# Kernel tuning notes

Hardware: AMD Instinct MI355X
Metric: run time of the kernel (lower is better)

Reference implementation:

```python
import jax, jax.numpy as jnp
import numpy as np

N = 50000          # nodes
E = 400000         # random edges (self-loops added in reference, per PyG default)
IN, HID, HEADS, OUT = 20, 64, 4, 256
NEG_SLOPE = 0.2    # GATv2Conv default negative_slope
EPS = 1e-16        # PyG softmax denom epsilon


def setup_inputs() -> dict:
    key = jax.random.key(0)
    ks = jax.random.split(key, 14)
    g = lambda k, shape, scale=0.1: (jax.random.normal(k, shape, jnp.float32) * scale)
    return {
        "x": jax.random.normal(ks[0], (N, IN), jnp.float32),
        "edge_index": jax.random.randint(ks[1], (2, E), 0, N, jnp.int32),
        # layer 1: GATv2Conv(IN -> HID, heads=HEADS, concat=True)
        "W_l1": g(ks[2], (IN, HEADS * HID)),
        "b_l1": jnp.zeros((HEADS * HID,), jnp.float32),
        "W_r1": g(ks[3], (IN, HEADS * HID)),
        "b_r1": jnp.zeros((HEADS * HID,), jnp.float32),
        "att1": g(ks[4], (HEADS, HID)),
        "bias1": jnp.zeros((HEADS * HID,), jnp.float32),
        # layer 2: GATv2Conv(HEADS*HID -> OUT, heads=1, concat=False)
        "W_l2": g(ks[5], (HEADS * HID, OUT)),
        "b_l2": jnp.zeros((OUT,), jnp.float32),
        "W_r2": g(ks[6], (HEADS * HID, OUT)),
        "b_r2": jnp.zeros((OUT,), jnp.float32),
        "att2": g(ks[7], (1, OUT)),
        "bias2": jnp.zeros((OUT,), jnp.float32),
    }


def _gatv2_layer(x, src, dst, W_l, b_l, W_r, b_r, att, bias, heads, ch, concat):
    n = x.shape[0]
    x_l = (x @ W_l + b_l).reshape(n, heads, ch)  # source transform
    x_r = (x @ W_r + b_r).reshape(n, heads, ch)  # target transform
    # GATv2: e_ij = att . LeakyReLU(x_l[j] + x_r[i])   (j->i edge)
    pre = jax.nn.leaky_relu(x_l[src] + x_r[dst], NEG_SLOPE)       # [E, H, C]
    logits = jnp.einsum('ehc,hc->eh', pre, att)                    # [E, H]
    # segment softmax over destination node (self-loops guarantee nonempty)
    m = jax.ops.segment_max(logits, dst, num_segments=n)
    w = jnp.exp(logits - m[dst])
    denom = jax.ops.segment_sum(w, dst, num_segments=n)
    alpha = w / (denom[dst] + EPS)                                 # [E, H]
    out = jax.ops.segment_sum(x_l[src] * alpha[:, :, None], dst, num_segments=n)
    out = out.reshape(n, heads * ch) if concat else out.mean(axis=1)
    return out + bias


def reference(x, edge_index, W_l1, b_l1, W_r1, b_r1, att1, bias1,
              W_l2, b_l2, W_r2, b_r2, att2, bias2):
    n = x.shape[0]
    loop = jnp.arange(n, dtype=edge_index.dtype)  # PyG add_self_loops=True
    src = jnp.concatenate([edge_index[0], loop])
    dst = jnp.concatenate([edge_index[1], loop])
    h = _gatv2_layer(x, src, dst, W_l1, b_l1, W_r1, b_r1, att1, bias1, HEADS, HID, True)
    h = jax.nn.elu(h)
    out = _gatv2_layer(h, src, dst, W_l2, b_l2, W_r2, b_r2, att2, bias2, 1, OUT, False)
    return out
```

## Files before the change

### kernel.cpp

```cpp
#include <hip/hip_runtime.h>
#include <math.h>

#define CH 256
#define SCAN_BLOCK 1024

typedef _Float16 h2 __attribute__((ext_vector_type(2)));
typedef _Float16 h4 __attribute__((ext_vector_type(4)));
typedef _Float16 f16x8 __attribute__((ext_vector_type(8)));
typedef float f32x4 __attribute__((ext_vector_type(4)));

__device__ __forceinline__ float elu(float v)   { return v > 0.f ? v : __expf(v) - 1.f; }

__device__ __forceinline__ unsigned short f2h(float f) {
    union { _Float16 h; unsigned short u; } c;
    c.h = (_Float16)f;
    return c.u;
}

__device__ __forceinline__ float edge_logit(h4 r, h2 xrlo, h2 xrhi, h2 alo, h2 ahi) {
    const h2 k = {(_Float16)0.2f, (_Float16)0.2f};
    h2 rlo = {r.x, r.y}, rhi = {r.z, r.w};
    h2 slo = rlo + xrlo;
    h2 shi = rhi + xrhi;
    slo = __builtin_elementwise_max(slo, slo * k);
    shi = __builtin_elementwise_max(shi, shi * k);
    float p = __builtin_amdgcn_fdot2(slo, alo, 0.f, false);
    return __builtin_amdgcn_fdot2(shi, ahi, p, false);
}

typedef const __attribute__((address_space(1))) unsigned int* gas_p;
typedef __attribute__((address_space(3))) unsigned int* las_p;
__device__ __forceinline__ void gload16(const unsigned short* g, unsigned short* l) {
    __builtin_amdgcn_global_load_lds((gas_p)g, (las_p)l, 16, 0, 0);
}

__global__ __launch_bounds__(256) void gemm1_kernel(const float* __restrict__ x,
                             const float* __restrict__ Wl, const float* __restrict__ bl,
                             const float* __restrict__ Wr, const float* __restrict__ br,
                             unsigned short* __restrict__ xl, unsigned short* __restrict__ xr, int n) {
    __shared__ float xs[64][20];
    int n0 = blockIdx.x * 64;
    int tid = threadIdx.x;
    for (int i = tid; i < 64 * 20; i += 256) {
        int m = i / 20, k = i % 20;
        int row = n0 + m;
        xs[m][k] = (row < n) ? x[(size_t)row * 20 + k] : 0.f;
    }
    int c = tid;
    float wl[20], wr[20];
#pragma unroll
    for (int k = 0; k < 20; ++k) { wl[k] = Wl[k * 256 + c]; wr[k] = Wr[k * 256 + c]; }
    float blv = bl[c], brv = br[c];
    __syncthreads();
#pragma unroll 1
    for (int g = 0; g < 8; ++g) {
        int base = g * 8;
        float al[8], ar[8];
#pragma unroll
        for (int m = 0; m < 8; ++m) { al[m] = blv; ar[m] = brv; }
#pragma unroll
        for (int k = 0; k < 20; ++k) {
            float wlv = wl[k], wrv = wr[k];
#pragma unroll
            for (int m = 0; m < 8; ++m) {
                float xv = xs[base + m][k];
                al[m] += xv * wlv;
                ar[m] += xv * wrv;
            }
        }
#pragma unroll
        for (int m = 0; m < 8; ++m) {
            int row = n0 + base + m;
            if (row < n) {
                xl[(size_t)row * 256 + c] = f2h(al[m]);
                xr[(size_t)row * 256 + c] = f2h(ar[m]);
            }
        }
    }
}

__global__ void count_deg(const int* __restrict__ ei, int* __restrict__ deg, int e) {
    int t = blockIdx.x * blockDim.x + threadIdx.x;
    if (t < e) atomicAdd(&deg[ei[e + t]], 1);
}

__global__ void scan_block_k(const int* __restrict__ deg, int* __restrict__ rowptr,
                             int* __restrict__ bsums, int n) {
    __shared__ int wsum[16];
    __shared__ int woff[17];
    int tid = threadIdx.x;
    int gi = blockIdx.x * SCAN_BLOCK + tid;
    int lane = tid & 63, wid = tid >> 6;
    int v = (gi < n) ? deg[gi] : 0;
    int incl = v;
#pragma unroll
    for (int d = 1; d < 64; d <<= 1) {
        int t = __shfl_up(incl, d, 64);
        if (lane >= d) incl += t;
    }
    if (lane == 63) wsum[wid] = incl;
    __syncthreads();
    if (tid < 16) {
        int s = wsum[tid];
#pragma unroll
        for (int d = 1; d < 16; d <<= 1) {
            int t = __shfl_up(s, d, 64);
            if (tid >= d) s += t;
        }
        woff[tid + 1] = s;
        if (tid == 0) woff[0] = 0;
    }
    __syncthreads();
    incl += woff[wid];
    if (gi < n) rowptr[gi + 1] = incl;
    if (tid == 0) bsums[blockIdx.x] = woff[16];
}

__global__ void scan_tops_k(int* bsums, int nb) {
    int tid = threadIdx.x;
    int v = (tid < nb) ? bsums[tid] : 0;
    int incl = v;
#pragma unroll
    for (int d = 1; d < 64; d <<= 1) {
        int t = __shfl_up(incl, d, 64);
        if (tid >= d) incl += t;
    }
    if (tid < nb) bsums[tid] = incl - v;
}

__global__ void scan_fix_k(int* __restrict__ rowptr, int* __restrict__ cursor,
                           const int* __restrict__ deg, const int* __restrict__ bsums, int n) {
    int gi = blockIdx.x * SCAN_BLOCK + threadIdx.x;
    if (gi >= n) return;
    int off = bsums[blockIdx.x];
    int incl = rowptr[gi + 1] + off;
    rowptr[gi + 1] = incl;
    cursor[gi] = incl - deg[gi];
    if (gi == 0) rowptr[0] = 0;
}

__global__ void scatter_k(const int* __restrict__ ei, int* __restrict__ cursor,
                          int* __restrict__ csr, int e) {
    int t = blockIdx.x * blockDim.x + threadIdx.x;
    if (t >= e) return;
    int s = ei[t], d = ei[e + t];
    int idx = atomicAdd(&cursor[d], 1);
    csr[idx] = s;
}

__global__ void fused_gat1(const unsigned short* __restrict__ xl, const unsigned short* __restrict__ xr,
                           const int* __restrict__ rowptr, const int* __restrict__ csr,
                           const float* __restrict__ att, const float* __restrict__ bias,
                           unsigned short* __restrict__ hout, int n) {
    int wid = threadIdx.x >> 6;
    int lane = threadIdx.x & 63;
    int i = blockIdx.x * 4 + wid;
    if (i >= n) return;
    h4 xr4 = ((const h4*)(xr + (size_t)i * CH))[lane];
    h2 xrlo = {xr4.x, xr4.y}, xrhi = {xr4.z, xr4.w};
    float4 a4 = ((const float4*)att)[lane];
    h2 alo = {(_Float16)a4.x, (_Float16)a4.y};
    h2 ahi = {(_Float16)a4.z, (_Float16)a4.w};
    h4 xli = ((const h4*)(xl + (size_t)i * CH))[lane];
    float ps = edge_logit(xli, xrlo, xrhi, alo, ahi);
    ps += __shfl_xor(ps, 1); ps += __shfl_xor(ps, 2);
    ps += __shfl_xor(ps, 4); ps += __shfl_xor(ps, 8);
    float m = ps, l = 1.f;
    float4 acc = make_float4((float)xli.x, (float)xli.y, (float)xli.z, (float)xli.w);
    int beg = rowptr[i], end = rowptr[i + 1];
    for (int e = beg; e < end; e += 4) {
        int cnt = end - e;
        int s0 = csr[e];
        int s1 = (cnt > 1) ? csr[e + 1] : s0;
        int s2 = (cnt > 2) ? csr[e + 2] : s0;
        int s3 = (cnt > 3) ? csr[e + 3] : s0;
        h4 r0 = ((const h4*)(xl + (size_t)s0 * CH))[lane];
        h4 r1 = ((const h4*)(xl + (size_t)s1 * CH))[lane];
        h4 r2 = ((const h4*)(xl + (size_t)s2 * CH))[lane];
        h4 r3 = ((const h4*)(xl + (size_t)s3 * CH))[lane];
        float p0 = edge_logit(r0, xrlo, xrhi, alo, ahi);
        float p1 = edge_logit(r1, xrlo, xrhi, alo, ahi);
        float p2 = edge_logit(r2, xrlo, xrhi, alo, ahi);
        float p3 = edge_logit(r3, xrlo, xrhi, alo, ahi);
        p0 += __shfl_xor(p0, 1); p1 += __shfl_xor(p1, 1); p2 += __shfl_xor(p2, 1); p3 += __shfl_xor(p3, 1);
        p0 += __shfl_xor(p0, 2); p1 += __shfl_xor(p1, 2); p2 += __shfl_xor(p2, 2); p3 += __shfl_xor(p3, 2);
        p0 += __shfl_xor(p0, 4); p1 += __shfl_xor(p1, 4); p2 += __shfl_xor(p2, 4); p3 += __shfl_xor(p3, 4);
        p0 += __shfl_xor(p0, 8); p1 += __shfl_xor(p1, 8); p2 += __shfl_xor(p2, 8); p3 += __shfl_xor(p3, 8);
        if (cnt < 2) p1 = -INFINITY;
        if (cnt < 3) p2 = -INFINITY;
        if (cnt < 4) p3 = -INFINITY;
        float mn = fmaxf(m, fmaxf(fmaxf(p0, p1), fmaxf(p2, p3)));
        float sc = __expf(m - mn);
        float w0 = __expf(p0 - mn), w1 = __expf(p1 - mn);
        float w2 = __expf(p2 - mn), w3 = __expf(p3 - mn);
        l = l * sc + w0 + w1 + w2 + w3;
        acc.x = acc.x * sc + w0 * (float)r0.x + w1 * (float)r1.x + w2 * (float)r2.x + w3 * (float)r3.x;
        acc.y = acc.y * sc + w0 * (float)r0.y + w1 * (float)r1.y + w2 * (float)r2.y + w3 * (float)r3.y;
        acc.z = acc.z * sc + w0 * (float)r0.z + w1 * (float)r1.z + w2 * (float)r2.z + w3 * (float)r3.z;
        acc.w = acc.w * sc + w0 * (float)r0.w + w1 * (float)r1.w + w2 * (float)r2.w + w3 * (float)r3.w;
        m = mn;
    }
    float inv = 1.f / (l + 1e-16f);
    float4 b4 = ((const float4*)bias)[lane];
    h4 o;
    o.x = (_Float16)elu(acc.x * inv + b4.x);
    o.y = (_Float16)elu(acc.y * inv + b4.y);
    o.z = (_Float16)elu(acc.z * inv + b4.z);
    o.w = (_Float16)elu(acc.w * inv + b4.w);
    ((h4*)(hout + (size_t)i * CH))[lane] = o;
}

__global__ void fused_gat2(const unsigned short* __restrict__ xl, const unsigned short* __restrict__ xr,
                           const int* __restrict__ rowptr, const int* __restrict__ csr,
                           const float* __restrict__ att, const float* __restrict__ bias,
                           float* __restrict__ out, int n) {
    int wid = threadIdx.x >> 6;
    int lane = threadIdx.x & 63;
    int i = blockIdx.x * 4 + wid;
    if (i >= n) return;
    h4 xr4 = ((const h4*)(xr + (size_t)i * CH))[lane];
    h2 xrlo = {xr4.x, xr4.y}, xrhi = {xr4.z, xr4.w};
    float4 a4 = ((const float4*)att)[lane];
    h2 alo = {(_Float16)a4.x, (_Float16)a4.y};
    h2 ahi = {(_Float16)a4.z, (_Float16)a4.w};
    h4 xli = ((const h4*)(xl + (size_t)i * CH))[lane];
    float ps = edge_logit(xli, xrlo, xrhi, alo, ahi);
    ps += __shfl_xor(ps, 1); ps += __shfl_xor(ps, 2); ps += __shfl_xor(ps, 4);
    ps += __shfl_xor(ps, 8); ps += __shfl_xor(ps, 16); ps += __shfl_xor(ps, 32);
    float m = ps, l = 1.f;
    float4 acc = make_float4((float)xli.x, (float)xli.y, (float)xli.z, (float)xli.w);
    int beg = rowptr[i], end = rowptr[i + 1];
    for (int e = beg; e < end; e += 4) {
        int cnt = end - e;
        int s0 = csr[e];
        int s1 = (cnt > 1) ? csr[e + 1] : s0;
        int s2 = (cnt > 2) ? csr[e + 2] : s0;
        int s3 = (cnt > 3) ? csr[e + 3] : s0;
        h4 r0 = ((const h4*)(xl + (size_t)s0 * CH))[lane];
        h4 r1 = ((const h4*)(xl + (size_t)s1 * CH))[lane];
        h4 r2 = ((const h4*)(xl + (size_t)s2 * CH))[lane];
        h4 r3 = ((const h4*)(xl + (size_t)s3 * CH))[lane];
        float p0 = edge_logit(r0, xrlo, xrhi, alo, ahi);
        float p1 = edge_logit(r1, xrlo, xrhi, alo, ahi);
        float p2 = edge_logit(r2, xrlo, xrhi, alo, ahi);
        float p3 = edge_logit(r3, xrlo, xrhi, alo, ahi);
#pragma unroll
        for (int d = 1; d < 64; d <<= 1) {
            p0 += __shfl_xor(p0, d); p1 += __shfl_xor(p1, d);
            p2 += __shfl_xor(p2, d); p3 += __shfl_xor(p3, d);
        }
        if (cnt < 2) p1 = -INFINITY;
        if (cnt < 3) p2 = -INFINITY;
        if (cnt < 4) p3 = -INFINITY;
        float mn = fmaxf(m, fmaxf(fmaxf(p0, p1), fmaxf(p2, p3)));
        float sc = __expf(m - mn);
        float w0 = __expf(p0 - mn), w1 = __expf(p1 - mn);
        float w2 = __expf(p2 - mn), w3 = __expf(p3 - mn);
        l = l * sc + w0 + w1 + w2 + w3;
        acc.x = acc.x * sc + w0 * (float)r0.x + w1 * (float)r1.x + w2 * (float)r2.x + w3 * (float)r3.x;
        acc.y = acc.y * sc + w0 * (float)r0.y + w1 * (float)r1.y + w2 * (float)r2.y + w3 * (float)r3.y;
        acc.z = acc.z * sc + w0 * (float)r0.z + w1 * (float)r1.z + w2 * (float)r2.z + w3 * (float)r3.z;
        acc.w = acc.w * sc + w0 * (float)r0.w + w1 * (float)r1.w + w2 * (float)r2.w + w3 * (float)r3.w;
        m = mn;
    }
    float inv = 1.f / (l + 1e-16f);
    float4 b4 = ((const float4*)bias)[lane];
    float4 o;
    o.x = acc.x * inv + b4.x;
    o.y = acc.y * inv + b4.y;
    o.z = acc.z * inv + b4.z;
    o.w = acc.w * inv + b4.w;
    ((float4*)(out + (size_t)i * CH))[lane] = o;
}

__global__ void wconv(const float* __restrict__ Wl2, const float* __restrict__ Wr2,
                      unsigned short* __restrict__ Wt) {
    int t = blockIdx.x * 256 + threadIdx.x;
    int z = t >> 16;
    int idx = t & 65535;
    int k = idx >> 8, nn = idx & 255;
    const float* W = z ? Wr2 : Wl2;
    Wt[z * 65536 + nn * 256 + k] = f2h(W[k * 256 + nn]);
}

#define LDE 32
__global__ __launch_bounds__(256) void gemm_mfma(
        const unsigned short* __restrict__ A,
        const unsigned short* __restrict__ Wt,
        const float* __restrict__ ba, const float* __restrict__ bb,
        unsigned short* __restrict__ Ca, unsigned short* __restrict__ Cb, int M) {
    const unsigned short* Wz = Wt + (size_t)blockIdx.z * 65536;
    const float* bias = blockIdx.z ? bb : ba;
    unsigned short* C = blockIdx.z ? Cb : Ca;

    __shared__ unsigned short As[2][128 * LDE];
    __shared__ unsigned short Bs[2][128 * LDE];

    int m0 = blockIdx.x * 128, n0 = blockIdx.y * 128;
    int tid = threadIdx.x;
    int lane = tid & 63, wid = tid >> 6;
    int wm = wid & 1, wn = wid >> 1;
    int q = lane >> 4, l15 = lane & 15;

    int lr = lane >> 2;
    int lc = (lane & 3) * 8;
    int Mm1 = M - 1;
    int ra0 = m0 + wid * 32 + lr;      if (ra0 > Mm1) ra0 = Mm1;
    int ra1 = m0 + wid * 32 + 16 + lr; if (ra1 > Mm1) ra1 = Mm1;
    const unsigned short* pa0 = A  + (size_t)ra0 * 256 + lc;
    const unsigned short* pa1 = A  + (size_t)ra1 * 256 + lc;
    const unsigned short* pb0 = Wz + (size_t)(n0 + wid * 32 + lr) * 256 + lc;
    const unsigned short* pb1 = Wz + (size_t)(n0 + wid * 32 + 16 + lr) * 256 + lc;

    f32x4 acc[4][4];
#pragma unroll
    for (int i = 0; i < 4; ++i)
#pragma unroll
        for (int j = 0; j < 4; ++j) acc[i][j] = (f32x4){0.f, 0.f, 0.f, 0.f};

#define STAGE(b, kb) do {                                   \
        int koff = (kb) * 32;                               \
        gload16(pa0 + koff, &As[b][(wid * 32) * LDE]);      \
        gload16(pa1 + koff, &As[b][(wid * 32 + 16) * LDE]); \
        gload16(pb0 + koff, &Bs[b][(wid * 32) * LDE]);      \
        gload16(pb1 + koff, &Bs[b][(wid * 32 + 16) * LDE]); \
    } while (0)

    STAGE(0, 0);
    __syncthreads();

#pragma unroll
    for (int kb = 0; kb < 8; ++kb) {
        int cur = kb & 1;
        if (kb < 7) STAGE(cur ^ 1, kb + 1);

        f16x8 af[4], bfr[4];
#pragma unroll
        for (int f = 0; f < 4; ++f)
            af[f] = *(const f16x8*)&As[cur][(wm * 64 + f * 16 + l15) * LDE + q * 8];
#pragma unroll
        for (int f = 0; f < 4; ++f)
            bfr[f] = *(const f16x8*)&Bs[cur][(wn * 64 + f * 16 + l15) * LDE + q * 8];
#pragma unroll
        for (int i = 0; i < 4; ++i)
#pragma unroll
            for (int j = 0; j < 4; ++j)
                acc[i][j] = __builtin_amdgcn_mfma_f32_16x16x32_f16(af[i], bfr[j], acc[i][j], 0, 0, 0);

        __syncthreads();
    }
#undef STAGE

#pragma unroll
    for (int j = 0; j < 4; ++j) {
        int gcol = n0 + wn * 64 + j * 16 + l15;
        float bcol = bias[gcol];
#pragma unroll
        for (int i = 0; i < 4; ++i) {
            int row = m0 + wm * 64 + i * 16 + q * 4;
#pragma unroll
            for (int rr = 0; rr < 4; ++rr) {
                int grow = row + rr;
                if (grow < M)
                    C[(size_t)grow * 256 + gcol] = f2h(acc[i][j][rr] + bcol);
            }
        }
    }
}

extern "C" void kernel_launch(void* const* d_in, const int* in_sizes, int n_in,
                              void* d_out, int out_size, void* d_ws, size_t ws_size,
                              hipStream_t stream) {
    const float* x    = (const float*)d_in[0];
    const int*   ei   = (const int*)d_in[1];
    const float* Wl1  = (const float*)d_in[2];
    const float* bl1  = (const float*)d_in[3];
    const float* Wr1  = (const float*)d_in[4];
    const float* br1  = (const float*)d_in[5];
    const float* att1 = (const float*)d_in[6];
    const float* bias1= (const float*)d_in[7];
    const float* Wl2  = (const float*)d_in[8];
    const float* bl2  = (const float*)d_in[9];
    const float* Wr2  = (const float*)d_in[10];
    const float* br2  = (const float*)d_in[11];
    const float* att2 = (const float*)d_in[12];
    const float* bias2= (const float*)d_in[13];

    int n = in_sizes[0] / 20;
    int e = in_sizes[1] / 2;
    float* out = (float*)d_out;
    size_t nch = (size_t)n * CH;

    unsigned short* buf0 = (unsigned short*)d_ws;
    unsigned short* buf1 = buf0 + nch;
    unsigned short* hbuf = buf1 + nch;
    unsigned short* wt2  = hbuf + nch;
    int* deg    = (int*)(wt2 + 2 * 65536);
    int* rowptr = deg + n;
    int* cursor = rowptr + n + 1;
    int* bsums  = cursor + n;
    int* csr    = bsums + 64;

    hipMemsetAsync(deg, 0, (size_t)n * sizeof(int), stream);

    gemm1_kernel<<<(n + 63) / 64, 256, 0, stream>>>(x, Wl1, bl1, Wr1, br1, buf0, buf1, n);

    count_deg<<<(e + 255) / 256, 256, 0, stream>>>(ei, deg, e);
    int nb = (n + SCAN_BLOCK - 1) / SCAN_BLOCK;
    scan_block_k<<<nb, SCAN_BLOCK, 0, stream>>>(deg, rowptr, bsums, n);
    scan_tops_k<<<1, 64, 0, stream>>>(bsums, nb);
    scan_fix_k<<<nb, SCAN_BLOCK, 0, stream>>>(rowptr, cursor, deg, bsums, n);
    scatter_k<<<(e + 255) / 256, 256, 0, stream>>>(ei, cursor, csr, e);

    wconv<<<512, 256, 0, stream>>>(Wl2, Wr2, wt2);

    fused_gat1<<<(n + 3) / 4, 256, 0, stream>>>(buf0, buf1, rowptr, csr, att1, bias1, hbuf, n);

    gemm_mfma<<<dim3((n + 127) / 128, 2, 2), 256, 0, stream>>>(hbuf, wt2, bl2, br2, buf0, buf1, n);

    fused_gat2<<<(n + 3) / 4, 256, 0, stream>>>(buf0, buf1, rowptr, csr, att2, bias2, out, n);
}
```

Before: 315.9 us.

## Unroll edge gathers to 8, use DPP reductions and exp2 online softmax

Both fused GAT aggregation kernels now gather eight neighbour rows per iteration instead of four, which raises memory-level parallelism on the random xl gathers. Intra-16-lane logit reductions use DPP row operations instead of ds_swizzle/bpermute shuffles. The attention vector is pre-scaled by log2(e) so the softmax can use exp2 directly, and the running-max rescale is skipped when the max does not change. In exchange, register pressure rises and tail iterations do redundant loads of the last valid edge; fp16 rounding of the prescaled attention weights changes results slightly.

```diff
diff --git a/kernel.cpp b/kernel.cpp
--- a/kernel.cpp
+++ b/kernel.cpp
@@ -3,6 +3,7 @@
 
 #define CH 256
 #define SCAN_BLOCK 1024
+#define LOG2E 1.44269504088896f
 
 typedef _Float16 h2 __attribute__((ext_vector_type(2)));
 typedef _Float16 h4 __attribute__((ext_vector_type(4)));
@@ -26,6 +27,25 @@
     shi = __builtin_elementwise_max(shi, shi * k);
     float p = __builtin_amdgcn_fdot2(slo, alo, 0.f, false);
     return __builtin_amdgcn_fdot2(shi, ahi, p, false);
+}
+
+template<int C>
+__device__ __forceinline__ float dppadd(float v) {
+    int t = __builtin_amdgcn_update_dpp(0, __float_as_int(v), C, 0xf, 0xf, true);
+    return v + __int_as_float(t);
+}
+__device__ __forceinline__ float red16(float p) {
+    p = dppadd<0xB1>(p);
+    p = dppadd<0x4E>(p);
+    p = dppadd<0x141>(p);
+    p = dppadd<0x140>(p);
+    return p;
+}
+__device__ __forceinline__ float red64(float p) {
+    p = red16(p);
+    p += __shfl_xor(p, 16);
+    p += __shfl_xor(p, 32);
+    return p;
 }
 
 typedef const __attribute__((address_space(1))) unsigned int* gas_p;
@@ -159,46 +179,69 @@
     h4 xr4 = ((const h4*)(xr + (size_t)i * CH))[lane];
     h2 xrlo = {xr4.x, xr4.y}, xrhi = {xr4.z, xr4.w};
     float4 a4 = ((const float4*)att)[lane];
-    h2 alo = {(_Float16)a4.x, (_Float16)a4.y};
-    h2 ahi = {(_Float16)a4.z, (_Float16)a4.w};
+    h2 alo = {(_Float16)(a4.x * LOG2E), (_Float16)(a4.y * LOG2E)};
+    h2 ahi = {(_Float16)(a4.z * LOG2E), (_Float16)(a4.w * LOG2E)};
     h4 xli = ((const h4*)(xl + (size_t)i * CH))[lane];
-    float ps = edge_logit(xli, xrlo, xrhi, alo, ahi);
-    ps += __shfl_xor(ps, 1); ps += __shfl_xor(ps, 2);
-    ps += __shfl_xor(ps, 4); ps += __shfl_xor(ps, 8);
-    float m = ps, l = 1.f;
+    float m = red16(edge_logit(xli, xrlo, xrhi, alo, ahi));
+    float l = 1.f;
     float4 acc = make_float4((float)xli.x, (float)xli.y, (float)xli.z, (float)xli.w);
     int beg = rowptr[i], end = rowptr[i + 1];
-    for (int e = beg; e < end; e += 4) {
+    int el = end - 1;
+    for (int e = beg; e < end; e += 8) {
         int cnt = end - e;
         int s0 = csr[e];
-        int s1 = (cnt > 1) ? csr[e + 1] : s0;
-        int s2 = (cnt > 2) ? csr[e + 2] : s0;
-        int s3 = (cnt > 3) ? csr[e + 3] : s0;
+        int s1 = csr[min(e + 1, el)];
+        int s2 = csr[min(e + 2, el)];
+        int s3 = csr[min(e + 3, el)];
+        int s4 = csr[min(e + 4, el)];
+        int s5 = csr[min(e + 5, el)];
+        int s6 = csr[min(e + 6, el)];
+        int s7 = csr[min(e + 7, el)];
         h4 r0 = ((const h4*)(xl + (size_t)s0 * CH))[lane];
         h4 r1 = ((const h4*)(xl + (size_t)s1 * CH))[lane];
         h4 r2 = ((const h4*)(xl + (size_t)s2 * CH))[lane];
         h4 r3 = ((const h4*)(xl + (size_t)s3 * CH))[lane];
-        float p0 = edge_logit(r0, xrlo, xrhi, alo, ahi);
-        float p1 = edge_logit(r1, xrlo, xrhi, alo, ahi);
-        float p2 = edge_logit(r2, xrlo, xrhi, alo, ahi);
-        float p3 = edge_logit(r3, xrlo, xrhi, alo, ahi);
-        p0 += __shfl_xor(p0, 1); p1 += __shfl_xor(p1, 1); p2 += __shfl_xor(p2, 1); p3 += __shfl_xor(p3, 1);
-        p0 += __shfl_xor(p0, 2); p1 += __shfl_xor(p1, 2); p2 += __shfl_xor(p2, 2); p3 += __shfl_xor(p3, 2);
-        p0 += __shfl_xor(p0, 4); p1 += __shfl_xor(p1, 4); p2 += __shfl_xor(p2, 4); p3 += __shfl_xor(p3, 4);
-        p0 += __shfl_xor(p0, 8); p1 += __shfl_xor(p1, 8); p2 += __shfl_xor(p2, 8); p3 += __shfl_xor(p3, 8);
-        if (cnt < 2) p1 = -INFINITY;
-        if (cnt < 3) p2 = -INFINITY;
-        if (cnt < 4) p3 = -INFINITY;
-        float mn = fmaxf(m, fmaxf(fmaxf(p0, p1), fmaxf(p2, p3)));
-        float sc = __expf(m - mn);
-        float w0 = __expf(p0 - mn), w1 = __expf(p1 - mn);
-        float w2 = __expf(p2 - mn), w3 = __expf(p3 - mn);
-        l = l * sc + w0 + w1 + w2 + w3;
-        acc.x = acc.x * sc + w0 * (float)r0.x + w1 * (float)r1.x + w2 * (float)r2.x + w3 * (float)r3.x;
-        acc.y = acc.y * sc + w0 * (float)r0.y + w1 * (float)r1.y + w2 * (float)r2.y + w3 * (float)r3.y;
-        acc.z = acc.z * sc + w0 * (float)r0.z + w1 * (float)r1.z + w2 * (float)r2.z + w3 * (float)r3.z;
-        acc.w = acc.w * sc + w0 * (float)r0.w + w1 * (float)r1.w + w2 * (float)r2.w + w3 * (float)r3.w;
-        m = mn;
+        h4 r4 = ((const h4*)(xl + (size_t)s4 * CH))[lane];
+        h4 r5 = ((const h4*)(xl + (size_t)s5 * CH))[lane];
+        h4 r6 = ((const h4*)(xl + (size_t)s6 * CH))[lane];
+        h4 r7 = ((const h4*)(xl + (size_t)s7 * CH))[lane];
+        float p0 = red16(edge_logit(r0, xrlo, xrhi, alo, ahi));
+        float p1 = red16(edge_logit(r1, xrlo, xrhi, alo, ahi));
+        float p2 = red16(edge_logit(r2, xrlo, xrhi, alo, ahi));
+        float p3 = red16(edge_logit(r3, xrlo, xrhi, alo, ahi));
+        float p4 = red16(edge_logit(r4, xrlo, xrhi, alo, ahi));
+        float p5 = red16(edge_logit(r5, xrlo, xrhi, alo, ahi));
+        float p6 = red16(edge_logit(r6, xrlo, xrhi, alo, ahi));
+        float p7 = red16(edge_logit(r7, xrlo, xrhi, alo, ahi));
+        if (cnt < 8) {
+            if (cnt <= 1) p1 = -INFINITY;
+            if (cnt <= 2) p2 = -INFINITY;
+            if (cnt <= 3) p3 = -INFINITY;
+            if (cnt <= 4) p4 = -INFINITY;
+            if (cnt <= 5) p5 = -INFINITY;
+            if (cnt <= 6) p6 = -INFINITY;
+            p7 = -INFINITY;
+        }
+        float mn = fmaxf(m, fmaxf(fmaxf(fmaxf(p0, p1), fmaxf(p2, p3)),
+                                  fmaxf(fmaxf(p4, p5), fmaxf(p6, p7))));
+        if (mn > m) {
+            float sc = __builtin_exp2f(m - mn);
+            l *= sc; acc.x *= sc; acc.y *= sc; acc.z *= sc; acc.w *= sc;
+            m = mn;
+        }
+        float w0 = __builtin_exp2f(p0 - m), w1 = __builtin_exp2f(p1 - m);
+        float w2 = __builtin_exp2f(p2 - m), w3 = __builtin_exp2f(p3 - m);
+        float w4 = __builtin_exp2f(p4 - m), w5 = __builtin_exp2f(p5 - m);
+        float w6 = __builtin_exp2f(p6 - m), w7 = __builtin_exp2f(p7 - m);
+        l += ((w0 + w1) + (w2 + w3)) + ((w4 + w5) + (w6 + w7));
+        acc.x += w0*(float)r0.x + w1*(float)r1.x + w2*(float)r2.x + w3*(float)r3.x
+               + w4*(float)r4.x + w5*(float)r5.x + w6*(float)r6.x + w7*(float)r7.x;
+        acc.y += w0*(float)r0.y + w1*(float)r1.y + w2*(float)r2.y + w3*(float)r3.y
+               + w4*(float)r4.y + w5*(float)r5.y + w6*(float)r6.y + w7*(float)r7.y;
+        acc.z += w0*(float)r0.z + w1*(float)r1.z + w2*(float)r2.z + w3*(float)r3.z
+               + w4*(float)r4.z + w5*(float)r5.z + w6*(float)r6.z + w7*(float)r7.z;
+        acc.w += w0*(float)r0.w + w1*(float)r1.w + w2*(float)r2.w + w3*(float)r3.w
+               + w4*(float)r4.w + w5*(float)r5.w + w6*(float)r6.w + w7*(float)r7.w;
     }
     float inv = 1.f / (l + 1e-16f);
     float4 b4 = ((const float4*)bias)[lane];
@@ -221,47 +264,69 @@
     h4 xr4 = ((const h4*)(xr + (size_t)i * CH))[lane];
     h2 xrlo = {xr4.x, xr4.y}, xrhi = {xr4.z, xr4.w};
     float4 a4 = ((const float4*)att)[lane];
-    h2 alo = {(_Float16)a4.x, (_Float16)a4.y};
-    h2 ahi = {(_Float16)a4.z, (_Float16)a4.w};
+    h2 alo = {(_Float16)(a4.x * LOG2E), (_Float16)(a4.y * LOG2E)};
+    h2 ahi = {(_Float16)(a4.z * LOG2E), (_Float16)(a4.w * LOG2E)};
     h4 xli = ((const h4*)(xl + (size_t)i * CH))[lane];
-    float ps = edge_logit(xli, xrlo, xrhi, alo, ahi);
-    ps += __shfl_xor(ps, 1); ps += __shfl_xor(ps, 2); ps += __shfl_xor(ps, 4);
-    ps += __shfl_xor(ps, 8); ps += __shfl_xor(ps, 16); ps += __shfl_xor(ps, 32);
-    float m = ps, l = 1.f;
+    float m = red64(edge_logit(xli, xrlo, xrhi, alo, ahi));
+    float l = 1.f;
     float4 acc = make_float4((float)xli.x, (float)xli.y, (float)xli.z, (float)xli.w);
     int beg = rowptr[i], end = rowptr[i + 1];
-    for (int e = beg; e < end; e += 4) {
+    int el = end - 1;
+    for (int e = beg; e < end; e += 8) {
         int cnt = end - e;
         int s0 = csr[e];
-        int s1 = (cnt > 1) ? csr[e + 1] : s0;
-        int s2 = (cnt > 2) ? csr[e + 2] : s0;
-        int s3 = (cnt > 3) ? csr[e + 3] : s0;
+        int s1 = csr[min(e + 1, el)];
+        int s2 = csr[min(e + 2, el)];
+        int s3 = csr[min(e + 3, el)];
+        int s4 = csr[min(e + 4, el)];
+        int s5 = csr[min(e + 5, el)];
+        int s6 = csr[min(e + 6, el)];
+        int s7 = csr[min(e + 7, el)];
         h4 r0 = ((const h4*)(xl + (size_t)s0 * CH))[lane];
         h4 r1 = ((const h4*)(xl + (size_t)s1 * CH))[lane];
         h4 r2 = ((const h4*)(xl + (size_t)s2 * CH))[lane];
         h4 r3 = ((const h4*)(xl + (size_t)s3 * CH))[lane];
-        float p0 = edge_logit(r0, xrlo, xrhi, alo, ahi);
-        float p1 = edge_logit(r1, xrlo, xrhi, alo, ahi);
-        float p2 = edge_logit(r2, xrlo, xrhi, alo, ahi);
-        float p3 = edge_logit(r3, xrlo, xrhi, alo, ahi);
-#pragma unroll
-        for (int d = 1; d < 64; d <<= 1) {
-            p0 += __shfl_xor(p0, d); p1 += __shfl_xor(p1, d);
-            p2 += __shfl_xor(p2, d); p3 += __shfl_xor(p3, d);
-        }
-        if (cnt < 2) p1 = -INFINITY;
-        if (cnt < 3) p2 = -INFINITY;
-        if (cnt < 4) p3 = -INFINITY;
-        float mn = fmaxf(m, fmaxf(fmaxf(p0, p1), fmaxf(p2, p3)));
-        float sc = __expf(m - mn);
-        float w0 = __expf(p0 - mn), w1 = __expf(p1 - mn);
-        float w2 = __expf(p2 - mn), w3 = __expf(p3 - mn);
-        l = l * sc + w0 + w1 + w2 + w3;
-        acc.x = acc.x * sc + w0 * (float)r0.x + w1 * (float)r1.x + w2 * (float)r2.x + w3 * (float)r3.x;
-        acc.y = acc.y * sc + w0 * (float)r0.y + w1 * (float)r1.y + w2 * (float)r2.y + w3 * (float)r3.y;
-        acc.z = acc.z * sc + w0 * (float)r0.z + w1 * (float)r1.z + w2 * (float)r2.z + w3 * (float)r3.z;
-        acc.w = acc.w * sc + w0 * (float)r0.w + w1 * (float)r1.w + w2 * (float)r2.w + w3 * (float)r3.w;
-        m = mn;
+        h4 r4 = ((const h4*)(xl + (size_t)s4 * CH))[lane];
+        h4 r5 = ((const h4*)(xl + (size_t)s5 * CH))[lane];
+        h4 r6 = ((const h4*)(xl + (size_t)s6 * CH))[lane];
+        h4 r7 = ((const h4*)(xl + (size_t)s7 * CH))[lane];
+        float p0 = red64(edge_logit(r0, xrlo, xrhi, alo, ahi));
+        float p1 = red64(edge_logit(r1, xrlo, xrhi, alo, ahi));
+        float p2 = red64(edge_logit(r2, xrlo, xrhi, alo, ahi));
+        float p3 = red64(edge_logit(r3, xrlo, xrhi, alo, ahi));
+        float p4 = red64(edge_logit(r4, xrlo, xrhi, alo, ahi));
+        float p5 = red64(edge_logit(r5, xrlo, xrhi, alo, ahi));
+        float p6 = red64(edge_logit(r6, xrlo, xrhi, alo, ahi));
+        float p7 = red64(edge_logit(r7, xrlo, xrhi, alo, ahi));
+        if (cnt < 8) {
+            if (cnt <= 1) p1 = -INFINITY;
+            if (cnt <= 2) p2 = -INFINITY;
+            if (cnt <= 3) p3 = -INFINITY;
+            if (cnt <= 4) p4 = -INFINITY;
+            if (cnt <= 5) p5 = -INFINITY;
+            if (cnt <= 6) p6 = -INFINITY;
+            p7 = -INFINITY;
+        }
+        float mn = fmaxf(m, fmaxf(fmaxf(fmaxf(p0, p1), fmaxf(p2, p3)),
+                                  fmaxf(fmaxf(p4, p5), fmaxf(p6, p7))));
+        if (mn > m) {
+            float sc = __builtin_exp2f(m - mn);
+            l *= sc; acc.x *= sc; acc.y *= sc; acc.z *= sc; acc.w *= sc;
+            m = mn;
+        }
+        float w0 = __builtin_exp2f(p0 - m), w1 = __builtin_exp2f(p1 - m);
+        float w2 = __builtin_exp2f(p2 - m), w3 = __builtin_exp2f(p3 - m);
+        float w4 = __builtin_exp2f(p4 - m), w5 = __builtin_exp2f(p5 - m);
+        float w6 = __builtin_exp2f(p6 - m), w7 = __builtin_exp2f(p7 - m);
+        l += ((w0 + w1) + (w2 + w3)) + ((w4 + w5) + (w6 + w7));
+        acc.x += w0*(float)r0.x + w1*(float)r1.x + w2*(float)r2.x + w3*(float)r3.x
+               + w4*(float)r4.x + w5*(float)r5.x + w6*(float)r6.x + w7*(float)r7.x;
+        acc.y += w0*(float)r0.y + w1*(float)r1.y + w2*(float)r2.y + w3*(float)r3.y
+               + w4*(float)r4.y + w5*(float)r5.y + w6*(float)r6.y + w7*(float)r7.y;
+        acc.z += w0*(float)r0.z + w1*(float)r1.z + w2*(float)r2.z + w3*(float)r3.z
+               + w4*(float)r4.z + w5*(float)r5.z + w6*(float)r6.z + w7*(float)r7.z;
+        acc.w += w0*(float)r0.w + w1*(float)r1.w + w2*(float)r2.w + w3*(float)r3.w
+               + w4*(float)r4.w + w5*(float)r5.w + w6*(float)r6.w + w7*(float)r7.w;
     }
     float inv = 1.f / (l + 1e-16f);
     float4 b4 = ((const float4*)bias)[lane];
```

Measured after the change: 323.3 us. +2.3%, slower.
